# Kernel optimization log

Measured on AMD Instinct MI355X. Metric: run time of the kernel, lower is better.

The kernel has to match this reference:

```python
import jax, jax.numpy as jnp
import numpy as np

EPS = 1e-20
TEMP = 0.07
PATCH = 64
STEP = 32  # patch_size * overlap(0.5)


def zero_softmax(x, eps=1e-5):
    # ZeroSoftmax: ((exp(x)-1)^2) / (sum + eps), maps x==0 -> exactly 0 weight
    e = jnp.square(jnp.exp(x) - 1.0)
    return e / (jnp.sum(e, axis=-1, keepdims=True) + eps)


def _scaling_mask(H, W, p, step):
    # constant overlap-count mask from CRW.compute_scaling_mask (static shapes)
    sm = np.zeros((H, W), np.float32)
    for i in range(0, H - step, step):
        for j in range(0, W - step, step):
            sm[i:i + p, j:j + p] += 1.0
    return jnp.asarray(sm)


def _window_sums(m, p, step):
    # m: (B,T,SP,H,W) -> sliding-window sums (B,T,SP,nH,nW) via integral image
    ii = jnp.cumsum(jnp.cumsum(m, axis=-2), axis=-1)
    ii = jnp.pad(ii, ((0, 0), (0, 0), (0, 0), (1, 0), (1, 0)))
    H = m.shape[-2]
    nH = (H - p) // step + 1
    lo = jnp.arange(nH) * step
    hi = lo + p
    r_hi = ii[..., hi, :]   # (B,T,SP,nH,W+1)
    r_lo = ii[..., lo, :]
    return r_hi[..., hi] - r_hi[..., lo] - r_lo[..., hi] + r_lo[..., lo]


def setup_inputs() -> dict:
    key = jax.random.key(0)
    k1, k2, k3 = jax.random.split(key, 3)
    B, T, H, W = 2, 4, 256, 256
    nH = (H - PATCH) // STEP + 1  # 7
    N = nH * nH                   # 49 patches
    Cenc, D, SP = 512, 128, 64
    feats = jax.random.normal(k1, (B, N, Cenc, T), jnp.float32)
    W_head = jax.random.normal(k2, (Cenc, D), jnp.float32) / np.sqrt(Cenc)
    sp_mask = jax.random.randint(k3, (B, T, H, W), 0, SP, jnp.int32)
    return {"feats": feats, "W_head": W_head, "sp_mask": sp_mask, "max_sp_num": SP}


def reference(feats, W_head, sp_mask, max_sp_num):
    B, N, Cenc, T = feats.shape
    H, W = sp_mask.shape[-2:]
    SP = max_sp_num

    # --- pixels_to_nodes tail: projection head + L2 normalize over channel dim ---
    q = jnp.einsum('bnct,cd->bndt', feats, W_head)            # (B,N,128,T)
    nrm = jnp.maximum(jnp.linalg.norm(q, axis=2, keepdims=True), 1e-12)
    q = q / nrm
    q = jnp.transpose(q, (0, 2, 3, 1))                        # (B,128,T,N)

    # --- patches_to_sp_embeddings: windowed superpixel pooling ---
    oh = (sp_mask[:, :, None, :, :] ==
          jnp.arange(SP, dtype=sp_mask.dtype)[None, None, :, None, None]
          ).astype(jnp.float32)                               # (B,T,SP,H,W)
    sm = _scaling_mask(H, W, PATCH, STEP)                     # (H,W)
    ws = _window_sums(oh / sm, PATCH, STEP)                   # (B,T,SP,nH,nW)
    denom = jnp.sum(oh, axis=(-1, -2)) + EPS                  # (B,T,SP)
    wts = jnp.transpose(ws, (0, 1, 3, 4, 2)) / denom[:, :, None, None, :]
    wts = wts.reshape(B, T, N, SP)                            # (B,T,N,SP)
    q_sp = jnp.einsum('bdtn,btns->bdts', q, wts)              # (B,128,T,SP)

    # --- affinity + zero_softmax stochastic matrices ---
    As = jnp.einsum('bdtn,bdtm->btnm', q_sp[:, :, :-1], q_sp[:, :, 1:])  # (B,T-1,SP,SP)
    A12 = zero_softmax(As / TEMP)
    A21 = zero_softmax(jnp.swapaxes(As, -1, -2) / TEMP)

    # --- palindrome random walks + cross-entropy to cycle-consistency targets ---
    tgt = jnp.tile(jnp.arange(SP), B)
    loss = jnp.float32(0.0)
    AAs = []
    for i in range(1, T - 1):
        mats = [A12[:, k] for k in range(i + 1)] + [A21[:, k] for k in range(i, -1, -1)]
        aa = mats[0]
        for m in mats[1:]:
            aa = aa @ m
        AAs.append(aa)
        logits = jnp.log(aa + EPS).reshape(B * SP, SP)
        logp = jax.nn.log_softmax(logits, axis=-1)
        loss = loss + jnp.mean(-logp[jnp.arange(B * SP), tgt])
    return loss, jnp.stack(AAs)
```

## Files before the change

kernel.cpp:

```cpp
#include <hip/hip_runtime.h>
#include <hip/hip_bf16.h>

constexpr int NWIN = 49;
constexpr int QLD  = 52;

constexpr int OFF_WS   = 0;
constexpr int OFF_Q    = 26624;
constexpr int OFF_QSP  = 79872;
constexpr int OFF_A12T = 169984;
constexpr int OFF_A21  = 194560;
constexpr int OFF_A21T = 219136;
constexpr int OFF_R1T  = 251904;
constexpr int OFF_L    = 260096;
constexpr int OFF_BAR  = 276480;

__global__ void __launch_bounds__(256, 1)
k_front(const int* __restrict__ mask, const float* __restrict__ feats,
        const float* __restrict__ Wh, float* __restrict__ ws, float* __restrict__ q) {
    if (blockIdx.x < 392) {
        int win = blockIdx.x % NWIN;
        int bt  = blockIdx.x / NWIN;
        int wy = win / 7, wx = win % 7;
        __shared__ float loc[64];
        if (threadIdx.x < 64) loc[threadIdx.x] = 0.f;
        __syncthreads();
        const int* base = mask + bt * 65536 + (wy * 32) * 256 + wx * 32;
        #pragma unroll
        for (int it = 0; it < 16; ++it) {
            int idx = it * 256 + (int)threadIdx.x;
            int r = idx >> 6, c = idx & 63;
            int s = base[r * 256 + c];
            int y = wy * 32 + r, x = wx * 32 + c;
            float w = 1.f;
            if (y >= 32 && y < 224) w *= 0.5f;
            if (x >= 32 && x < 224) w *= 0.5f;
            atomicAdd(&loc[s], w);
        }
        __syncthreads();
        if (threadIdx.x < 64) {
            ws[(bt * 64 + (int)threadIdx.x) * QLD + win] = loc[threadIdx.x];
        } else if (win == 0) {
            int s = threadIdx.x & 63;
            int col = 49 + (int)(threadIdx.x >> 6) - 1;
            ws[(bt * 64 + s) * QLD + col] = 0.f;
        }
    } else {
        int bid = blockIdx.x - 392;
        int n = bid % NWIN, b = bid / NWIN;
        __shared__ float4 f4[512];
        __shared__ float4 psum4[512];
        __shared__ float4 red4[2];
        const float4* fp4 = (const float4*)(feats + (size_t)(b * NWIN + n) * 2048);
        for (int i = threadIdx.x; i < 512; i += 256) f4[i] = fp4[i];
        __syncthreads();

        int dl = threadIdx.x & 63, ch = threadIdx.x >> 6;
        float a0 = 0.f, a1 = 0.f, a2 = 0.f, a3 = 0.f;
        float b0 = 0.f, b1 = 0.f, b2 = 0.f, b3 = 0.f;
        const float* wpa = Wh + dl;
        const float* wpb = Wh + dl + 64;
        int c0 = ch * 128;
        #pragma unroll 8
        for (int c = c0; c < c0 + 128; ++c) {
            float w0 = wpa[c * 128];
            float w1 = wpb[c * 128];
            float4 fv = f4[c];
            a0 += fv.x * w0; a1 += fv.y * w0; a2 += fv.z * w0; a3 += fv.w * w0;
            b0 += fv.x * w1; b1 += fv.y * w1; b2 += fv.z * w1; b3 += fv.w * w1;
        }
        psum4[ch * 128 + dl]      = make_float4(a0, a1, a2, a3);
        psum4[ch * 128 + dl + 64] = make_float4(b0, b1, b2, b3);
        __syncthreads();

        float4 A;
        if (threadIdx.x < 128) {
            float4 p0 = psum4[threadIdx.x],       p1 = psum4[128 + threadIdx.x];
            float4 p2 = psum4[256 + threadIdx.x], p3 = psum4[384 + threadIdx.x];
            A = make_float4((p0.x + p1.x) + (p2.x + p3.x),
                            (p0.y + p1.y) + (p2.y + p3.y),
                            (p0.z + p1.z) + (p2.z + p3.z),
                            (p0.w + p1.w) + (p2.w + p3.w));
            float sx = A.x * A.x, sy = A.y * A.y, sz = A.z * A.z, sw = A.w * A.w;
            for (int off = 32; off; off >>= 1) {
                sx += __shfl_down(sx, off); sy += __shfl_down(sy, off);
                sz += __shfl_down(sz, off); sw += __shfl_down(sw, off);
            }
            if ((threadIdx.x & 63) == 0) red4[threadIdx.x >> 6] = make_float4(sx, sy, sz, sw);
        }
        __syncthreads();
        if (threadIdx.x < 128) {
            float4 r0 = red4[0], r1 = red4[1];
            float ix = 1.f / fmaxf(sqrtf(r0.x + r1.x), 1e-12f);
            float iy = 1.f / fmaxf(sqrtf(r0.y + r1.y), 1e-12f);
            float iz = 1.f / fmaxf(sqrtf(r0.z + r1.z), 1e-12f);
            float iw = 1.f / fmaxf(sqrtf(r0.w + r1.w), 1e-12f);
            float* qb = q + (size_t)(b * 128 + (int)threadIdx.x) * 4 * QLD + n;
            qb[0 * QLD] = A.x * ix;
            qb[1 * QLD] = A.y * iy;
            qb[2 * QLD] = A.z * iz;
            qb[3 * QLD] = A.w * iw;
        }
    }
}

__global__ void k_qsp(const float* __restrict__ q, const float* __restrict__ wsg,
                      float* __restrict__ qsp, float* __restrict__ out,
                      int* __restrict__ bar) {
    if (blockIdx.x == 0 && threadIdx.x < 4) {
        bar[threadIdx.x] = 0;
        if (threadIdx.x == 0) out[0] = 0.f;
    }
    int gid = blockIdx.x * 256 + threadIdx.x;
    int d = gid & 127;
    int s = (gid >> 7) & 63;
    int t = (gid >> 13) & 3;
    int b = gid >> 15;
    const float4* qrow = (const float4*)(q + (size_t)((b * 128 + d) * 4 + t) * QLD);
    const float4* wrow = (const float4*)(wsg + (size_t)((b * 4 + t) * 64 + s) * QLD);
    float acc = 0.f, den = 0.f;
    #pragma unroll
    for (int i = 0; i < 13; ++i) {
        float4 w = wrow[i];
        float4 qv = qrow[i];
        den += w.x + w.y + w.z + w.w;
        acc += qv.x * w.x + qv.y * w.y + qv.z * w.z + qv.w * w.w;
    }
    int w = (s * 32 + ((d >> 2) ^ (s & 31))) * 4 + (d & 3);
    qsp[(size_t)(b * 4 + t) * 8192 + w] = acc / (den + 1e-20f);
}


__device__ __forceinline__ void dump_mat(float* M, const float4* v) {
    #pragma unroll
    for (int it = 0; it < 4; ++it) {
        int idx = it * 256 + (int)threadIdx.x;
        int r = idx >> 4, c4 = (idx & 15) << 2;
        *(float4*)&M[r * 64 + (c4 ^ ((r & 15) << 2))] = v[it];
    }
}

__device__ __forceinline__ void stage1(float* M, const float* __restrict__ G) {
    const float4* g = (const float4*)G;
    float4 v[4];
    #pragma unroll
    for (int it = 0; it < 4; ++it) v[it] = g[it * 256 + (int)threadIdx.x];
    dump_mat(M, v);
}

__device__ __forceinline__ void mm256_sw(float* acc, const float* Ra, const float* Rb) {
    int tid = threadIdx.x;
    int nl = tid >> 4, ml = tid & 15;
    int sxa = nl << 2, sxb = ml << 2;
    #pragma unroll
    for (int i = 0; i < 16; ++i) acc[i] = 0.f;
    #pragma unroll 4
    for (int k0 = 0; k0 < 64; k0 += 4) {
        float4 av[4], bv[4];
        #pragma unroll
        for (int i = 0; i < 4; ++i)
            av[i] = *(const float4*)&Ra[(nl + 16 * i) * 64 + (k0 ^ sxa)];
        #pragma unroll
        for (int j = 0; j < 4; ++j)
            bv[j] = *(const float4*)&Rb[(ml + 16 * j) * 64 + (k0 ^ sxb)];
        #pragma unroll
        for (int i = 0; i < 4; ++i)
            #pragma unroll
            for (int j = 0; j < 4; ++j)
                acc[i * 4 + j] += av[i].x * bv[j].x + av[i].y * bv[j].y
                                + av[i].z * bv[j].z + av[i].w * bv[j].w;
    }
}

__device__ __forceinline__ void wr256_sw(float* M, const float* acc) {
    int nl = threadIdx.x >> 4, ml = threadIdx.x & 15;
    #pragma unroll
    for (int i = 0; i < 4; ++i)
        #pragma unroll
        for (int j = 0; j < 4; ++j) {
            int r = nl + 16 * i, k = ml + 16 * j;
            M[r * 64 + (((k & ~3) ^ ((r & 15) << 2)) | (k & 3))] = acc[i * 4 + j];
        }
}

__device__ __forceinline__ void store_mat(float* __restrict__ G, const float* acc) {
    int nl = threadIdx.x >> 4, ml = threadIdx.x & 15;
    #pragma unroll
    for (int i = 0; i < 4; ++i)
        #pragma unroll
        for (int j = 0; j < 4; ++j)
            G[(nl + 16 * i) * 64 + ml + 16 * j] = acc[i * 4 + j];
}

__device__ __forceinline__ void store_loss(const float* acc, float* __restrict__ aa,
                                           float* __restrict__ out, float* red) {
    int tid = threadIdx.x;
    int nl = tid >> 4, ml = tid & 15;
    #pragma unroll
    for (int i = 0; i < 4; ++i)
        #pragma unroll
        for (int j = 0; j < 4; ++j)
            aa[(nl + 16 * i) * 64 + (ml + 16 * j)] = acc[i * 4 + j];
    int l = tid & 63;
    float part = 0.f;
    #pragma unroll
    for (int i = 0; i < 4; ++i) {
        float rsum = acc[i * 4 + 0] + acc[i * 4 + 1] + acc[i * 4 + 2] + acc[i * 4 + 3];
        rsum += __shfl_down(rsum, 8, 16);
        rsum += __shfl_down(rsum, 4, 16);
        rsum += __shfl_down(rsum, 2, 16);
        rsum += __shfl_down(rsum, 1, 16);
        float dv = __shfl(acc[5 * i], (l & 48) | nl, 64);
        if ((l & 15) == 0) part += logf(rsum + 6.4e-19f) - logf(dv + 1e-20f);
    }
    for (int off = 32; off; off >>= 1) part += __shfl_down(part, off);
    if (l == 0) red[tid >> 6] = part;
    __syncthreads();
    if (tid == 0) atomicAdd(out, (red[0] + red[1] + red[2] + red[3]) * (1.f / 128.f));
}

__device__ __forceinline__ void gbar(int* cnt, int target) {
    __syncthreads();
    if (threadIdx.x == 0) {
        __threadfence();
        __hip_atomic_fetch_add(cnt, 1, __ATOMIC_ACQ_REL, __HIP_MEMORY_SCOPE_AGENT);
        while (__hip_atomic_load(cnt, __ATOMIC_ACQUIRE, __HIP_MEMORY_SCOPE_AGENT) < target)
            __builtin_amdgcn_s_sleep(2);
        __threadfence();
    }
    __syncthreads();
}

__global__ void __launch_bounds__(256, 1)
k_tail(const float* __restrict__ qsp,
       float* __restrict__ a12T, float* __restrict__ a21, float* __restrict__ a21T,
       float* __restrict__ wsR1T, float* __restrict__ wsL,
       float* __restrict__ out, int* __restrict__ bar) {
    __shared__ float SM[16384];
    float* M0 = SM;
    float* M1 = SM + 4096;
    float* M2 = SM + 8192;
    float* M3 = SM + 12288;
    const int tid = threadIdx.x;
    const int blk = blockIdx.x;
    const int t = blk % 3, b = blk / 3;

    {
        float4* qaT4 = (float4*)SM;
        float4* qbT4 = (float4*)SM + 2048;
        {
            const float4* gA = (const float4*)(qsp + (size_t)(b * 4 + t) * 8192);
            const float4* gB = (const float4*)(qsp + (size_t)(b * 4 + t + 1) * 8192);
            #pragma unroll
            for (int it = 0; it < 8; ++it) {
                int idx = it * 256 + tid;
                qaT4[idx] = gA[idx];
                qbT4[idx] = gB[idx];
            }
        }
        __syncthreads();

        const int nl = tid >> 4, ml = tid & 15;
        float acc[16];
        #pragma unroll
        for (int i = 0; i < 16; ++i) acc[i] = 0.f;
        #pragma unroll 8
        for (int k4 = 0; k4 < 32; ++k4) {
            float4 av[4], bv[4];
            #pragma unroll
            for (int i = 0; i < 4; ++i) { int n = nl + 16 * i; av[i] = qaT4[n * 32 + (k4 ^ (n & 31))]; }
            #pragma unroll
            for (int j = 0; j < 4; ++j) { int m = ml + 16 * j; bv[j] = qbT4[m * 32 + (k4 ^ (m & 31))]; }
            #pragma unroll
            for (int i = 0; i < 4; ++i)
                #pragma unroll
                for (int j = 0; j < 4; ++j)
                    acc[i * 4 + j] += av[i].x * bv[j].x + av[i].y * bv[j].y
                                    + av[i].z * bv[j].z + av[i].w * bv[j].w;
        }
        __syncthreads();

        float* eb = (float*)qaT4;
        float* rs = (float*)qbT4;
        float* cs = rs + 64;
        #pragma unroll
        for (int i = 0; i < 4; ++i)
            #pragma unroll
            for (int j = 0; j < 4; ++j) {
                int n = nl + 16 * i, m = ml + 16 * j;
                float x = acc[i * 4 + j] * (1.f / 0.07f);
                float e = expf(x) - 1.f;
                eb[n * 65 + m] = e * e;
            }
        __syncthreads();
        if (tid < 128) {
            int r = tid & 63; bool isrow = tid < 64;
            float a = 0.f;
            #pragma unroll
            for (int k = 0; k < 64; ++k) a += isrow ? eb[r * 65 + k] : eb[k * 65 + r];
            (isrow ? rs : cs)[r] = a + 1e-5f;
        }
        __syncthreads();
        float* p12T = a12T + (b * 3 + t) * 4096;
        float* p21  = a21  + (b * 3 + t) * 4096;
        float* p21T = a21T + (b * 3 + t) * 4096;
        #pragma unroll
        for (int i = 0; i < 4; ++i)
            #pragma unroll
            for (int j = 0; j < 4; ++j) {
                int n = nl + 16 * i, m = ml + 16 * j;
                float v   = eb[n * 65 + m];
                float v12 = v / rs[n];
                float v21 = v / cs[m];
                if (t == 0) {
                    M3[n * 64 + (((m & ~3) ^ ((n & 15) << 2)) | (m & 3))] = v12;
                    p21T[n * 64 + m] = v21;
                } else if (t == 1) {
                    p12T[m * 64 + n] = v12;
                    M3[m * 64 + (((n & ~3) ^ ((m & 15) << 2)) | (n & 3))] = v21;
                } else {
                    p12T[m * 64 + n] = v12;
                    p21 [m * 64 + n] = v21;
                }
            }
    }
    gbar(bar + 0, 6);
    if (t == 2) return;
    const bool odd = (t == 1);

    if (!odd) {
        stage1(M0, a12T + (b * 3 + 1) * 4096);
        __syncthreads();
        float accP[16];
        mm256_sw(accP, M3, M0);
        wr256_sw(M1, accP);
        stage1(M2, a12T + (b * 3 + 2) * 4096);
        __syncthreads();
        float accL[16];
        mm256_sw(accL, M1, M2);
        store_mat(wsL + b * 4096, accL);
    } else {
        stage1(M0, a21T + (b * 3 + 0) * 4096);
        __syncthreads();
        float accR[16];
        mm256_sw(accR, M0, M3);
        store_mat(wsR1T + b * 4096, accR);
        wr256_sw(M1, accR);
        stage1(M2, a21 + (b * 3 + 2) * 4096);
        __syncthreads();
        float accRT[16];
        mm256_sw(accRT, M1, M2);
        wr256_sw(M0, accRT);
    }
    gbar(bar + 1, 4);

    if (!odd) {
        stage1(M2, wsR1T + b * 4096);
        __syncthreads();
        float acc[16];
        mm256_sw(acc, M1, M2);
        store_loss(acc, out + 1 + b * 4096, out, M0);
    } else {
        stage1(M2, wsL + b * 4096);
        __syncthreads();
        float acc[16];
        mm256_sw(acc, M2, M0);
        store_loss(acc, out + 1 + (2 + b) * 4096, out, M1);
    }
}

extern "C" void kernel_launch(void* const* d_in, const int* in_sizes, int n_in,
                              void* d_out, int out_size, void* d_ws, size_t ws_size,
                              hipStream_t stream) {
    const float* feats = (const float*)d_in[0];
    const float* Wh    = (const float*)d_in[1];
    const int*   mask  = (const int*)d_in[2];
    float* out = (float*)d_out;
    float* ws  = (float*)d_ws;

    float* ws_sums = ws + OFF_WS;
    float* q       = ws + OFF_Q;
    float* qsp     = ws + OFF_QSP;
    float* a12T    = ws + OFF_A12T;
    float* a21     = ws + OFF_A21;
    float* a21T    = ws + OFF_A21T;
    float* wsR1T   = ws + OFF_R1T;
    float* wsL     = ws + OFF_L;
    int*   bar     = (int*)(ws + OFF_BAR);

    k_front<<<392 + 2 * NWIN, 256, 0, stream>>>(mask, feats, Wh, ws_sums, q);
    k_qsp<<<256, 256, 0, stream>>>(q, ws_sums, qsp, out, bar);
    k_tail<<<6, 256, 0, stream>>>(qsp, a12T, a21, a21T,
                                  wsR1T, wsL, out, bar);
}
```

Before: 105.8 us.

## Replace overlapping window histograms with per-cell histograms and restructure projection GEMV

Superpixel pooling now builds a histogram per non-overlapping 32x32 cell (512 blocks) and reconstructs each 64x64 window's weighted counts in k_qsp by combining four cells with the overlap weights. This removes the 4x redundant mask reads and atomics of overlapping windows. The projection head loop is reorganized so each thread loads float4 of W_head and computes 4 output dims over 64 channels, with 8 partial sums reduced through padded shared memory. It adds gather work in k_qsp and more blocks in k_front.

```diff
diff --git a/kernel.cpp b/kernel.cpp
--- a/kernel.cpp
+++ b/kernel.cpp
@@ -4,7 +4,6 @@
 constexpr int NWIN = 49;
 constexpr int QLD  = 52;
 
-constexpr int OFF_WS   = 0;
 constexpr int OFF_Q    = 26624;
 constexpr int OFF_QSP  = 79872;
 constexpr int OFF_A12T = 169984;
@@ -13,73 +12,53 @@
 constexpr int OFF_R1T  = 251904;
 constexpr int OFF_L    = 260096;
 constexpr int OFF_BAR  = 276480;
+constexpr int OFF_H    = 276608;
 
 __global__ void __launch_bounds__(256, 1)
 k_front(const int* __restrict__ mask, const float* __restrict__ feats,
-        const float* __restrict__ Wh, float* __restrict__ ws, float* __restrict__ q) {
-    if (blockIdx.x < 392) {
-        int win = blockIdx.x % NWIN;
-        int bt  = blockIdx.x / NWIN;
-        int wy = win / 7, wx = win % 7;
-        __shared__ float loc[64];
-        if (threadIdx.x < 64) loc[threadIdx.x] = 0.f;
-        __syncthreads();
-        const int* base = mask + bt * 65536 + (wy * 32) * 256 + wx * 32;
-        #pragma unroll
-        for (int it = 0; it < 16; ++it) {
-            int idx = it * 256 + (int)threadIdx.x;
-            int r = idx >> 6, c = idx & 63;
-            int s = base[r * 256 + c];
-            int y = wy * 32 + r, x = wx * 32 + c;
-            float w = 1.f;
-            if (y >= 32 && y < 224) w *= 0.5f;
-            if (x >= 32 && x < 224) w *= 0.5f;
-            atomicAdd(&loc[s], w);
-        }
-        __syncthreads();
-        if (threadIdx.x < 64) {
-            ws[(bt * 64 + (int)threadIdx.x) * QLD + win] = loc[threadIdx.x];
-        } else if (win == 0) {
-            int s = threadIdx.x & 63;
-            int col = 49 + (int)(threadIdx.x >> 6) - 1;
-            ws[(bt * 64 + s) * QLD + col] = 0.f;
-        }
-    } else {
-        int bid = blockIdx.x - 392;
+        const float* __restrict__ Wh, float* __restrict__ h, float* __restrict__ q) {
+    if (blockIdx.x < 98) {
+        int bid = blockIdx.x;
         int n = bid % NWIN, b = bid / NWIN;
         __shared__ float4 f4[512];
-        __shared__ float4 psum4[512];
+        __shared__ float4 psum4[8 * 129];
         __shared__ float4 red4[2];
         const float4* fp4 = (const float4*)(feats + (size_t)(b * NWIN + n) * 2048);
         for (int i = threadIdx.x; i < 512; i += 256) f4[i] = fp4[i];
         __syncthreads();
 
-        int dl = threadIdx.x & 63, ch = threadIdx.x >> 6;
-        float a0 = 0.f, a1 = 0.f, a2 = 0.f, a3 = 0.f;
-        float b0 = 0.f, b1 = 0.f, b2 = 0.f, b3 = 0.f;
-        const float* wpa = Wh + dl;
-        const float* wpb = Wh + dl + 64;
-        int c0 = ch * 128;
+        int dl = threadIdx.x & 31, ch = threadIdx.x >> 5;
+        const float4* wh4 = (const float4*)Wh;
+        float a0x=0.f,a0y=0.f,a0z=0.f,a0w=0.f;
+        float a1x=0.f,a1y=0.f,a1z=0.f,a1w=0.f;
+        float a2x=0.f,a2y=0.f,a2z=0.f,a2w=0.f;
+        float a3x=0.f,a3y=0.f,a3z=0.f,a3w=0.f;
+        int c0 = ch * 64;
         #pragma unroll 8
-        for (int c = c0; c < c0 + 128; ++c) {
-            float w0 = wpa[c * 128];
-            float w1 = wpb[c * 128];
+        for (int cc = 0; cc < 64; ++cc) {
+            int c = c0 + cc;
+            float4 w4 = wh4[c * 32 + dl];
             float4 fv = f4[c];
-            a0 += fv.x * w0; a1 += fv.y * w0; a2 += fv.z * w0; a3 += fv.w * w0;
-            b0 += fv.x * w1; b1 += fv.y * w1; b2 += fv.z * w1; b3 += fv.w * w1;
-        }
-        psum4[ch * 128 + dl]      = make_float4(a0, a1, a2, a3);
-        psum4[ch * 128 + dl + 64] = make_float4(b0, b1, b2, b3);
+            a0x += fv.x * w4.x; a0y += fv.y * w4.x; a0z += fv.z * w4.x; a0w += fv.w * w4.x;
+            a1x += fv.x * w4.y; a1y += fv.y * w4.y; a1z += fv.z * w4.y; a1w += fv.w * w4.y;
+            a2x += fv.x * w4.z; a2y += fv.y * w4.z; a2z += fv.z * w4.z; a2w += fv.w * w4.z;
+            a3x += fv.x * w4.w; a3y += fv.y * w4.w; a3z += fv.z * w4.w; a3w += fv.w * w4.w;
+        }
+        psum4[ch * 129 + dl * 4 + 0] = make_float4(a0x, a0y, a0z, a0w);
+        psum4[ch * 129 + dl * 4 + 1] = make_float4(a1x, a1y, a1z, a1w);
+        psum4[ch * 129 + dl * 4 + 2] = make_float4(a2x, a2y, a2z, a2w);
+        psum4[ch * 129 + dl * 4 + 3] = make_float4(a3x, a3y, a3z, a3w);
         __syncthreads();
 
         float4 A;
         if (threadIdx.x < 128) {
-            float4 p0 = psum4[threadIdx.x],       p1 = psum4[128 + threadIdx.x];
-            float4 p2 = psum4[256 + threadIdx.x], p3 = psum4[384 + threadIdx.x];
-            A = make_float4((p0.x + p1.x) + (p2.x + p3.x),
-                            (p0.y + p1.y) + (p2.y + p3.y),
-                            (p0.z + p1.z) + (p2.z + p3.z),
-                            (p0.w + p1.w) + (p2.w + p3.w));
+            int d = threadIdx.x;
+            A = psum4[d];
+            #pragma unroll
+            for (int c = 1; c < 8; ++c) {
+                float4 p = psum4[c * 129 + d];
+                A.x += p.x; A.y += p.y; A.z += p.z; A.w += p.w;
+            }
             float sx = A.x * A.x, sy = A.y * A.y, sz = A.z * A.z, sw = A.w * A.w;
             for (int off = 32; off; off >>= 1) {
                 sx += __shfl_down(sx, off); sy += __shfl_down(sy, off);
@@ -100,33 +79,79 @@
             qb[2 * QLD] = A.z * iz;
             qb[3 * QLD] = A.w * iw;
         }
-    }
-}
-
-__global__ void k_qsp(const float* __restrict__ q, const float* __restrict__ wsg,
+    } else {
+        int blkc = blockIdx.x - 98;
+        int bt = blkc >> 6, cell = blkc & 63;
+        int cy = cell >> 3, cx = cell & 7;
+        __shared__ float loc[64];
+        if (threadIdx.x < 64) loc[threadIdx.x] = 0.f;
+        __syncthreads();
+        const int* base = mask + bt * 65536 + (cy * 32) * 256 + cx * 32;
+        #pragma unroll
+        for (int it = 0; it < 4; ++it) {
+            int idx = it * 256 + (int)threadIdx.x;
+            int r = idx >> 5, c = idx & 31;
+            int s = base[r * 256 + c];
+            atomicAdd(&loc[s], 1.f);
+        }
+        __syncthreads();
+        if (threadIdx.x < 64)
+            h[(size_t)(bt * 64 + cell) * 64 + threadIdx.x] = loc[threadIdx.x];
+    }
+}
+
+__global__ void k_qsp(const float* __restrict__ q, const float* __restrict__ hg,
                       float* __restrict__ qsp, float* __restrict__ out,
                       int* __restrict__ bar) {
     if (blockIdx.x == 0 && threadIdx.x < 4) {
         bar[threadIdx.x] = 0;
         if (threadIdx.x == 0) out[0] = 0.f;
     }
-    int gid = blockIdx.x * 256 + threadIdx.x;
-    int d = gid & 127;
-    int s = (gid >> 7) & 63;
-    int t = (gid >> 13) & 3;
-    int b = gid >> 15;
+    int gid0 = blockIdx.x * 256;
+    int t = (gid0 >> 13) & 3;
+    int b = gid0 >> 15;
+    int bt = b * 4 + t;
+    int sbase = (gid0 >> 7) & 63;
+
+    __shared__ float wrow[2][52];
+    {
+        int grp = threadIdx.x >> 7;
+        int w = threadIdx.x & 127;
+        if (w < 52) {
+            float v = 0.f;
+            if (w < 49) {
+                int wy = w / 7, wx = w % 7;
+                int s = sbase + grp;
+                const float* hb = hg + (size_t)bt * 4096 + s;
+                float wr0 = (wy >= 1 && wy <= 6) ? 0.5f : 1.f;
+                float wr1 = (wy <= 5) ? 0.5f : 1.f;
+                float wc0 = (wx >= 1 && wx <= 6) ? 0.5f : 1.f;
+                float wc1 = (wx <= 5) ? 0.5f : 1.f;
+                v = wr0 * wc0 * hb[(wy * 8 + wx) * 64]
+                  + wr0 * wc1 * hb[(wy * 8 + wx + 1) * 64]
+                  + wr1 * wc0 * hb[((wy + 1) * 8 + wx) * 64]
+                  + wr1 * wc1 * hb[((wy + 1) * 8 + wx + 1) * 64];
+            }
+            wrow[grp][w] = v;
+        }
+    }
+    __syncthreads();
+
+    int tid = gid0 + threadIdx.x;
+    int d = tid & 127;
+    int s = (tid >> 7) & 63;
     const float4* qrow = (const float4*)(q + (size_t)((b * 128 + d) * 4 + t) * QLD);
-    const float4* wrow = (const float4*)(wsg + (size_t)((b * 4 + t) * 64 + s) * QLD);
+    const float4* wr4 = (const float4*)wrow[threadIdx.x >> 7];
     float acc = 0.f, den = 0.f;
     #pragma unroll
     for (int i = 0; i < 13; ++i) {
-        float4 w = wrow[i];
+        float4 w = wr4[i];
         float4 qv = qrow[i];
         den += w.x + w.y + w.z + w.w;
         acc += qv.x * w.x + qv.y * w.y + qv.z * w.z + qv.w * w.w;
     }
     int w = (s * 32 + ((d >> 2) ^ (s & 31))) * 4 + (d & 3);
-    qsp[(size_t)(b * 4 + t) * 8192 + w] = acc / (den + 1e-20f);
+    qsp[(size_t)bt * 8192 + w] = acc / (den + 1e-20f);
 }
 
 
@@ -377,7 +402,6 @@
     float* out = (float*)d_out;
     float* ws  = (float*)d_ws;
 
-    float* ws_sums = ws + OFF_WS;
     float* q       = ws + OFF_Q;
     float* qsp     = ws + OFF_QSP;
     float* a12T    = ws + OFF_A12T;
@@ -385,10 +409,11 @@
     float* a21T    = ws + OFF_A21T;
     float* wsR1T   = ws + OFF_R1T;
     float* wsL     = ws + OFF_L;
+    float* h       = ws + OFF_H;
     int*   bar     = (int*)(ws + OFF_BAR);
 
-    k_front<<<392 + 2 * NWIN, 256, 0, stream>>>(mask, feats, Wh, ws_sums, q);
-    k_qsp<<<256, 256, 0, stream>>>(q, ws_sums, qsp, out, bar);
+    k_front<<<98 + 512, 256, 0, stream>>>(mask, feats, Wh, h, q);
+    k_qsp<<<256, 256, 0, stream>>>(q, h, qsp, out, bar);
     k_tail<<<6, 256, 0, stream>>>(qsp, a12T, a21, a21T,
                                   wsR1T, wsL, out, bar);
 }
```

Result: faster. 100.1 us (-5.3%).
